# Performance work log

Hardware: AMD Instinct MI355X
Metric: run time of the kernel (lower is better)

## Reference

```python
import jax, jax.numpy as jnp
import numpy as np

B, S, D = 2, 2048, 2560
H, DH = 32, 80           # heads, head_size = D // H
RD = 32                  # rotary_dim (partial RoPE)
NI = 10240               # n_inner = 4 * n_embd
EPS = 1e-5
ROPE_BASE = 10000.0


def setup_inputs() -> dict:
    key = jax.random.key(0)
    ks = jax.random.split(key, 12)
    sd = 0.02
    inp = {
        "position_ids": jnp.broadcast_to(jnp.arange(S, dtype=jnp.int64), (B, S)),
        "hidden_states": jax.random.normal(ks[0], (B, S, D), jnp.float32),
        "ln_g": jnp.ones((D,), jnp.float32),
        "ln_b": jnp.zeros((D,), jnp.float32),
        "wqkv": jax.random.normal(ks[1], (D, 3 * D), jnp.float32) * sd,
        "bqkv": jnp.zeros((3 * D,), jnp.float32),
        "wout": jax.random.normal(ks[2], (D, D), jnp.float32) * sd,
        "bout": jnp.zeros((D,), jnp.float32),
        "wfc1": jax.random.normal(ks[3], (D, NI), jnp.float32) * sd,
        "bfc1": jnp.zeros((NI,), jnp.float32),
        "wfc2": jax.random.normal(ks[4], (NI, D), jnp.float32) * sd,
        "bfc2": jnp.zeros((D,), jnp.float32),
    }
    return inp


def _rope_neox(x, positions):
    # x: [B,S,H,DH]; apply neox-style rotary to first RD dims only
    half = RD // 2
    inv_freq = 1.0 / (ROPE_BASE ** (jnp.arange(0, RD, 2, dtype=jnp.float32) / RD))  # [half]
    ang = positions.astype(jnp.float32)[..., None] * inv_freq                        # [B,S,half]
    cos = jnp.cos(ang)[:, :, None, :]  # [B,S,1,half]
    sin = jnp.sin(ang)[:, :, None, :]
    x1 = x[..., :half]
    x2 = x[..., half:RD]
    rot = jnp.concatenate([x1 * cos - x2 * sin, x2 * cos + x1 * sin], axis=-1)
    return jnp.concatenate([rot, x[..., RD:]], axis=-1)


def reference(position_ids, hidden_states, ln_g, ln_b, wqkv, bqkv, wout, bout,
              wfc1, bfc1, wfc2, bfc2):
    residual = hidden_states
    # LayerNorm
    mu = jnp.mean(hidden_states, axis=-1, keepdims=True)
    var = jnp.mean(jnp.square(hidden_states - mu), axis=-1, keepdims=True)
    x = (hidden_states - mu) * jax.lax.rsqrt(var + EPS) * ln_g + ln_b

    # QKV projection
    qkv = x @ wqkv + bqkv
    q, k, v = jnp.split(qkv, 3, axis=-1)
    q = q.reshape(B, S, H, DH)
    k = k.reshape(B, S, H, DH)
    v = v.reshape(B, S, H, DH)

    # partial RoPE (neox style) on q and k
    q = _rope_neox(q, position_ids)
    k = _rope_neox(k, position_ids)

    # causal attention
    scale = DH ** -0.5
    scores = jnp.einsum("bqhd,bkhd->bhqk", q, k) * scale
    causal = jnp.tril(jnp.ones((S, S), jnp.bool_))
    scores = jnp.where(causal, scores, jnp.finfo(scores.dtype).min)
    probs = jax.nn.softmax(scores, axis=-1)
    attn = jnp.einsum("bhqk,bkhd->bqhd", probs, v).reshape(B, S, D)
    attn_out = attn @ wout + bout

    # MLP (gelu_new = tanh-approx gelu) on the SAME normed x (parallel residual)
    mlp = jax.nn.gelu(x @ wfc1 + bfc1, approximate=True) @ wfc2 + bfc2

    return attn_out + mlp + residual
```

## Files before the change

kernel.cpp:

```cpp
#include <hip/hip_runtime.h>

#define SS   2048
#define DD   2560
#define HH   32
#define DHH  80
#define DPAD 96
#define NII  10240
#define NTOK 4096

typedef __attribute__((ext_vector_type(8))) __bf16 bf16x8;
typedef __attribute__((ext_vector_type(4))) float  f32x4;

__device__ __forceinline__ float bf2f(unsigned short h) {
  union { unsigned u; float f; } c; c.u = ((unsigned)h) << 16; return c.f;
}
__device__ __forceinline__ unsigned short f2bf(float f) {
  union { float f; unsigned u; } c; c.f = f;
  unsigned r = c.u + 0x7FFFu + ((c.u >> 16) & 1u);
  return (unsigned short)(r >> 16);
}

__device__ __forceinline__ void gl_lds16(const void* gptr, void* lptr) {
  __builtin_amdgcn_global_load_lds((__attribute__((address_space(1))) void*)gptr,
                                   (__attribute__((address_space(3))) void*)lptr,
                                   16, 0, 0);
}

__global__ __launch_bounds__(256) void wt_transpose(const float* __restrict__ W,
                                                    unsigned short* __restrict__ Wt,
                                                    int K, int N) {
  __shared__ float tile[32][33];
  const int tx = threadIdx.x & 31, ty = threadIdx.x >> 5;
  const int n0 = blockIdx.x * 32, k0 = blockIdx.y * 32;
#pragma unroll
  for (int i = 0; i < 32; i += 8)
    tile[ty + i][tx] = W[(size_t)(k0 + ty + i) * N + n0 + tx];
  __syncthreads();
#pragma unroll
  for (int i = 0; i < 32; i += 8)
    Wt[(size_t)(n0 + ty + i) * K + k0 + tx] = f2bf(tile[tx][ty + i]);
}

__global__ __launch_bounds__(256) void ln_kernel(const float* __restrict__ X,
                                                 const float* __restrict__ G,
                                                 const float* __restrict__ Bb,
                                                 unsigned short* __restrict__ Xo) {
  const int row = blockIdx.x;
  const float4* xr = (const float4*)(X + (size_t)row * DD);
  float s = 0.f, ss = 0.f;
  for (int i = threadIdx.x; i < DD / 4; i += 256) {
    float4 v = xr[i];
    s  += v.x + v.y + v.z + v.w;
    ss += v.x * v.x + v.y * v.y + v.z * v.z + v.w * v.w;
  }
#pragma unroll
  for (int o = 32; o > 0; o >>= 1) { s += __shfl_down(s, o, 64); ss += __shfl_down(ss, o, 64); }
  __shared__ float red[8];
  const int w = threadIdx.x >> 6;
  if ((threadIdx.x & 63) == 0) { red[w] = s; red[4 + w] = ss; }
  __syncthreads();
  if (threadIdx.x == 0) {
    float ts  = red[0] + red[1] + red[2] + red[3];
    float tss = red[4] + red[5] + red[6] + red[7];
    float mu  = ts * (1.f / DD);
    float var = tss * (1.f / DD) - mu * mu;
    red[0] = mu; red[1] = rsqrtf(var + 1e-5f);
  }
  __syncthreads();
  const float mu = red[0], rstd = red[1];
  const float4* gr = (const float4*)G;
  const float4* br = (const float4*)Bb;
  for (int i = threadIdx.x; i < DD / 4; i += 256) {
    float4 v = xr[i], g = gr[i], b = br[i];
    ushort4 o;
    o.x = f2bf((v.x - mu) * rstd * g.x + b.x);
    o.y = f2bf((v.y - mu) * rstd * g.y + b.y);
    o.z = f2bf((v.z - mu) * rstd * g.z + b.z);
    o.w = f2bf((v.w - mu) * rstd * g.w + b.w);
    *(ushort4*)&Xo[(size_t)row * DD + i * 4] = o;
  }
}

__global__ __launch_bounds__(256) void rope_kernel(const unsigned short* __restrict__ qkv,
                                                   unsigned short* __restrict__ Qp,
                                                   unsigned short* __restrict__ Kp,
                                                   unsigned short* __restrict__ Vt) {
  const int tok = blockIdx.x;
  const int b = tok / SS, s = tok % SS;
  __shared__ float cs[16], sn[16];
  if (threadIdx.x < 16) {
    float inv = powf(10000.f, -(float)threadIdx.x / 16.f);
    float ang = (float)s * inv;
    cs[threadIdx.x] = cosf(ang);
    sn[threadIdx.x] = sinf(ang);
  }
  __syncthreads();
  const unsigned short* row = qkv + (size_t)tok * (3 * DD);
  for (int idx = threadIdx.x; idx < 2 * HH * DPAD; idx += 256) {
    const int which = idx / (HH * DPAD);
    const int rrem  = idx % (HH * DPAD);
    const int h = rrem / DPAD, d = rrem % DPAD;
    float val = 0.f;
    if (d < DHH) {
      const unsigned short* base = row + which * DD + h * DHH;
      if (d < 16) {
        float x1 = bf2f(base[d]), x2 = bf2f(base[d + 16]);
        val = x1 * cs[d] - x2 * sn[d];
      } else if (d < 32) {
        int i2 = d - 16;
        float x1 = bf2f(base[i2]), x2 = bf2f(base[d]);
        val = x2 * cs[i2] + x1 * sn[i2];
      } else {
        val = bf2f(base[d]);
      }
    }
    unsigned short* outp = which ? Kp : Qp;
    outp[(((size_t)b * HH + h) * SS + s) * DPAD + d] = f2bf(val);
  }
  for (int idx = threadIdx.x; idx < DD; idx += 256) {
    const int h = idx / DHH, d = idx % DHH;
    Vt[(((size_t)b * HH + h) * DHH + d) * SS + s] = row[2 * DD + idx];
  }
}

__global__ __launch_bounds__(128) void attn_kernel(const unsigned short* __restrict__ Qp,
                                                   const unsigned short* __restrict__ Kp,
                                                   const unsigned short* __restrict__ Vt,
                                                   unsigned short* __restrict__ O) {
  const int bid = blockIdx.x;
  const int bh = bid & 63;
  const int p = 63 - (bid >> 6);
  const int w = threadIdx.x >> 6;
  const int tile = p * 2 + w;
  const int lane = threadIdx.x & 63;
  const int lr = lane & 15, lg = lane >> 4;
  const int q0 = tile * 16;
  const unsigned short* Qh = Qp + (size_t)bh * SS * DPAD;
  const unsigned short* Kh = Kp + (size_t)bh * SS * DPAD;
  const unsigned short* Vh = Vt + (size_t)bh * DHH * SS;
  __shared__ __align__(16) char Plds[2][2048];
  char* Pb = Plds[w];

  bf16x8 qf[3];
#pragma unroll
  for (int c = 0; c < 3; ++c)
    qf[c] = *(const bf16x8*)&Qh[(size_t)(q0 + lr) * DPAD + c * 32 + lg * 8];

  f32x4 oacc[5];
#pragma unroll
  for (int d = 0; d < 5; ++d) oacc[d] = (f32x4){0.f, 0.f, 0.f, 0.f};
  float mrow[4], lrow[4];
#pragma unroll
  for (int r = 0; r < 4; ++r) { mrow[r] = -1e30f; lrow[r] = 0.f; }

  const float scl = 0.11180339887498949f;
  const int nt = q0 / 64 + 1;
  for (int t = 0; t < nt; ++t) {
    const int kv0 = t * 64;
    f32x4 s0 = (f32x4){0.f, 0.f, 0.f, 0.f};
    f32x4 s1 = (f32x4){0.f, 0.f, 0.f, 0.f};
    f32x4 s2 = (f32x4){0.f, 0.f, 0.f, 0.f};
    f32x4 s3 = (f32x4){0.f, 0.f, 0.f, 0.f};
#pragma unroll
    for (int c = 0; c < 3; ++c) {
      bf16x8 k0 = *(const bf16x8*)&Kh[(size_t)(kv0 +      lr) * DPAD + c * 32 + lg * 8];
      bf16x8 k1 = *(const bf16x8*)&Kh[(size_t)(kv0 + 16 + lr) * DPAD + c * 32 + lg * 8];
      bf16x8 k2 = *(const bf16x8*)&Kh[(size_t)(kv0 + 32 + lr) * DPAD + c * 32 + lg * 8];
      bf16x8 k3 = *(const bf16x8*)&Kh[(size_t)(kv0 + 48 + lr) * DPAD + c * 32 + lg * 8];
      s0 = __builtin_amdgcn_mfma_f32_16x16x32_bf16(qf[c], k0, s0, 0, 0, 0);
      s1 = __builtin_amdgcn_mfma_f32_16x16x32_bf16(qf[c], k1, s1, 0, 0, 0);
      s2 = __builtin_amdgcn_mfma_f32_16x16x32_bf16(qf[c], k2, s2, 0, 0, 0);
      s3 = __builtin_amdgcn_mfma_f32_16x16x32_bf16(qf[c], k3, s3, 0, 0, 0);
    }
    float pv0[4], pv1[4], pv2[4], pv3[4], mx[4];
    bool need = false;
#pragma unroll
    for (int r = 0; r < 4; ++r) {
      const int qr = q0 + lg * 4 + r;
      float a0 = (kv0 +      lr > qr) ? -1e30f : s0[r] * scl;
      float a1 = (kv0 + 16 + lr > qr) ? -1e30f : s1[r] * scl;
      float a2 = (kv0 + 32 + lr > qr) ? -1e30f : s2[r] * scl;
      float a3 = (kv0 + 48 + lr > qr) ? -1e30f : s3[r] * scl;
      pv0[r] = a0; pv1[r] = a1; pv2[r] = a2; pv3[r] = a3;
      float m = fmaxf(fmaxf(a0, a1), fmaxf(a2, a3));
#pragma unroll
      for (int mk = 1; mk < 16; mk <<= 1) m = fmaxf(m, __shfl_xor(m, mk, 64));
      mx[r] = m;
      need = need || (m > mrow[r] + 8.f);
    }
    if (__ballot(need)) {
#pragma unroll
      for (int r = 0; r < 4; ++r) {
        float mnew = fmaxf(mrow[r], mx[r]);
        float resc = __expf(mrow[r] - mnew);
        lrow[r] *= resc;
#pragma unroll
        for (int d = 0; d < 5; ++d) oacc[d][r] *= resc;
        mrow[r] = mnew;
      }
    }
#pragma unroll
    for (int r = 0; r < 4; ++r) {
      const int row = lg * 4 + r;
      const int swz = (row & 7) << 4;
      float p0 = __expf(pv0[r] - mrow[r]);
      float p1 = __expf(pv1[r] - mrow[r]);
      float p2 = __expf(pv2[r] - mrow[r]);
      float p3 = __expf(pv3[r] - mrow[r]);
      *(unsigned short*)(Pb + row * 128 + ((( 0 + lr) * 2) ^ swz)) = f2bf(p0);
      *(unsigned short*)(Pb + row * 128 + (((16 + lr) * 2) ^ swz)) = f2bf(p1);
      *(unsigned short*)(Pb + row * 128 + (((32 + lr) * 2) ^ swz)) = f2bf(p2);
      *(unsigned short*)(Pb + row * 128 + (((48 + lr) * 2) ^ swz)) = f2bf(p3);
      float rs = (p0 + p1) + (p2 + p3);
#pragma unroll
      for (int mk = 1; mk < 16; mk <<= 1) rs += __shfl_xor(rs, mk, 64);
      lrow[r] += rs;
    }
    asm volatile("s_waitcnt lgkmcnt(0)" ::: "memory");
    const int rswz = (lr & 7) << 4;
    bf16x8 pa0 = *(const bf16x8*)(Pb + lr * 128 + ((lg * 16) ^ rswz));
    bf16x8 pa1 = *(const bf16x8*)(Pb + lr * 128 + ((64 + lg * 16) ^ rswz));
#pragma unroll
    for (int d = 0; d < 5; ++d) {
      bf16x8 v0 = *(const bf16x8*)&Vh[(size_t)(d * 16 + lr) * SS + kv0 + lg * 8];
      bf16x8 v1 = *(const bf16x8*)&Vh[(size_t)(d * 16 + lr) * SS + kv0 + 32 + lg * 8];
      oacc[d] = __builtin_amdgcn_mfma_f32_16x16x32_bf16(pa0, v0, oacc[d], 0, 0, 0);
      oacc[d] = __builtin_amdgcn_mfma_f32_16x16x32_bf16(pa1, v1, oacc[d], 0, 0, 0);
    }
  }
  const int b = bh >> 5, h = bh & 31;
#pragma unroll
  for (int r = 0; r < 4; ++r) {
    const int qr = q0 + lg * 4 + r;
    const float inv = 1.f / lrow[r];
#pragma unroll
    for (int d = 0; d < 5; ++d)
      O[(size_t)(b * SS + qr) * DD + h * DHH + d * 16 + lr] = f2bf(oacc[d][r] * inv);
  }
}

__device__ __forceinline__ float gelu_f(float x) {
  float x3 = x * x * x;
  return 0.5f * x * (1.f + tanhf(0.7978845608028654f * (x + 0.044715f * x3)));
}

template <int MODE>
__global__ __launch_bounds__(512, 2) void gemm256(const unsigned short* __restrict__ A,
                                                  const unsigned short* __restrict__ Bt,
                                                  const float* __restrict__ bias,
                                                  void* __restrict__ Cout,
                                                  const unsigned short* __restrict__ addb,
                                                  const float* __restrict__ addf,
                                                  int M, int N, int K, int nbx) {
  __shared__ __align__(16) unsigned short smem[65536];
  char* ldsB = (char*)smem;

  const int nwg = gridDim.x;
  const int orig = blockIdx.x;
  const int qq = nwg >> 3, rr = nwg & 7;
  const int xcd = orig & 7, loc = orig >> 3;
  const int swz = (xcd < rr ? xcd * (qq + 1) : rr * (qq + 1) + (xcd - rr) * qq) + loc;
  const int by = swz / nbx, bx = swz % nbx;
  const int m0 = by * 256, n0 = bx * 256;

  const int tid = threadIdx.x;
  const int w = tid >> 6, lane = tid & 63;
  const int lr = lane & 15, lg = lane >> 4;
  const int wm = w & 1, wn = w >> 1;

  const int srow = w * 32 + (lane >> 2);
  const int sslot = ((lane & 3) ^ ((lane >> 3) & 3)) * 8;
  const unsigned short* aS0 = A  + (size_t)(m0 + srow) * K + sslot;
  const unsigned short* aS1 = A  + (size_t)(m0 + srow + 16) * K + sslot;
  const unsigned short* bS0 = Bt + (size_t)(n0 + srow) * K + sslot;
  const unsigned short* bS1 = Bt + (size_t)(n0 + srow + 16) * K + sslot;
  const int adest = w * 2048;

  const int fslot = ((lg ^ ((lr >> 1) & 3)) << 4);
  const int arow = wm * 128 + lr;
  const int brow = wn * 64 + lr;

  f32x4 acc[8][4];
#pragma unroll
  for (int i = 0; i < 8; ++i)
#pragma unroll
    for (int j = 0; j < 4; ++j) acc[i][j] = (f32x4){0.f, 0.f, 0.f, 0.f};

  const int nt = K >> 5;

#define STAGE_A(t)                                                        \
  { int _b = (t) & 3;                                                     \
    gl_lds16(aS0 + (size_t)(t) * 32, ldsB + _b * 16384 + adest);          \
    gl_lds16(aS1 + (size_t)(t) * 32, ldsB + _b * 16384 + adest + 1024); }
#define STAGE_B(t)                                                        \
  { int _b = (t) & 3;                                                     \
    gl_lds16(bS0 + (size_t)(t) * 32, ldsB + 65536 + _b * 16384 + adest);  \
    gl_lds16(bS1 + (size_t)(t) * 32, ldsB + 65536 + _b * 16384 + adest + 1024); }
#define LDA(t, m) (*(const bf16x8*)(ldsB + ((t) & 3) * 16384 + (arow + (m) * 16) * 64 + fslot))
#define LDB(t, n) (*(const bf16x8*)(ldsB + 65536 + ((t) & 3) * 16384 + (brow + (n) * 16) * 64 + fslot))

  STAGE_A(0); STAGE_B(0);
  STAGE_A(1); STAGE_B(1);
  STAGE_A(2); STAGE_B(2);
  asm volatile("s_waitcnt vmcnt(8)" ::: "memory");
  __builtin_amdgcn_s_barrier();
  __builtin_amdgcn_sched_barrier(0);

  for (int t = 0; t < nt; ++t) {
    bf16x8 b0 = LDB(t, 0), b1 = LDB(t, 1), b2 = LDB(t, 2), b3 = LDB(t, 3);
    bf16x8 a0 = LDA(t, 0), a1 = LDA(t, 1), a2 = LDA(t, 2), a3 = LDA(t, 3);
    if (t + 3 < nt) STAGE_A(t + 3);
    __builtin_amdgcn_s_barrier();
    __builtin_amdgcn_s_setprio(1);
    acc[0][0] = __builtin_amdgcn_mfma_f32_16x16x32_bf16(a0, b0, acc[0][0], 0, 0, 0);
    acc[0][1] = __builtin_amdgcn_mfma_f32_16x16x32_bf16(a0, b1, acc[0][1], 0, 0, 0);
    acc[0][2] = __builtin_amdgcn_mfma_f32_16x16x32_bf16(a0, b2, acc[0][2], 0, 0, 0);
    acc[0][3] = __builtin_amdgcn_mfma_f32_16x16x32_bf16(a0, b3, acc[0][3], 0, 0, 0);
    acc[1][0] = __builtin_amdgcn_mfma_f32_16x16x32_bf16(a1, b0, acc[1][0], 0, 0, 0);
    acc[1][1] = __builtin_amdgcn_mfma_f32_16x16x32_bf16(a1, b1, acc[1][1], 0, 0, 0);
    acc[1][2] = __builtin_amdgcn_mfma_f32_16x16x32_bf16(a1, b2, acc[1][2], 0, 0, 0);
    acc[1][3] = __builtin_amdgcn_mfma_f32_16x16x32_bf16(a1, b3, acc[1][3], 0, 0, 0);
    acc[2][0] = __builtin_amdgcn_mfma_f32_16x16x32_bf16(a2, b0, acc[2][0], 0, 0, 0);
    acc[2][1] = __builtin_amdgcn_mfma_f32_16x16x32_bf16(a2, b1, acc[2][1], 0, 0, 0);
    acc[2][2] = __builtin_amdgcn_mfma_f32_16x16x32_bf16(a2, b2, acc[2][2], 0, 0, 0);
    acc[2][3] = __builtin_amdgcn_mfma_f32_16x16x32_bf16(a2, b3, acc[2][3], 0, 0, 0);
    acc[3][0] = __builtin_amdgcn_mfma_f32_16x16x32_bf16(a3, b0, acc[3][0], 0, 0, 0);
    acc[3][1] = __builtin_amdgcn_mfma_f32_16x16x32_bf16(a3, b1, acc[3][1], 0, 0, 0);
    acc[3][2] = __builtin_amdgcn_mfma_f32_16x16x32_bf16(a3, b2, acc[3][2], 0, 0, 0);
    acc[3][3] = __builtin_amdgcn_mfma_f32_16x16x32_bf16(a3, b3, acc[3][3], 0, 0, 0);
    __builtin_amdgcn_s_setprio(0);
    __builtin_amdgcn_s_barrier();
    a0 = LDA(t, 4); a1 = LDA(t, 5); a2 = LDA(t, 6); a3 = LDA(t, 7);
    if (t + 3 < nt) STAGE_B(t + 3);
    __builtin_amdgcn_s_barrier();
    __builtin_amdgcn_s_setprio(1);
    acc[4][0] = __builtin_amdgcn_mfma_f32_16x16x32_bf16(a0, b0, acc[4][0], 0, 0, 0);
    acc[4][1] = __builtin_amdgcn_mfma_f32_16x16x32_bf16(a0, b1, acc[4][1], 0, 0, 0);
    acc[4][2] = __builtin_amdgcn_mfma_f32_16x16x32_bf16(a0, b2, acc[4][2], 0, 0, 0);
    acc[4][3] = __builtin_amdgcn_mfma_f32_16x16x32_bf16(a0, b3, acc[4][3], 0, 0, 0);
    acc[5][0] = __builtin_amdgcn_mfma_f32_16x16x32_bf16(a1, b0, acc[5][0], 0, 0, 0);
    acc[5][1] = __builtin_amdgcn_mfma_f32_16x16x32_bf16(a1, b1, acc[5][1], 0, 0, 0);
    acc[5][2] = __builtin_amdgcn_mfma_f32_16x16x32_bf16(a1, b2, acc[5][2], 0, 0, 0);
    acc[5][3] = __builtin_amdgcn_mfma_f32_16x16x32_bf16(a1, b3, acc[5][3], 0, 0, 0);
    acc[6][0] = __builtin_amdgcn_mfma_f32_16x16x32_bf16(a2, b0, acc[6][0], 0, 0, 0);
    acc[6][1] = __builtin_amdgcn_mfma_f32_16x16x32_bf16(a2, b1, acc[6][1], 0, 0, 0);
    acc[6][2] = __builtin_amdgcn_mfma_f32_16x16x32_bf16(a2, b2, acc[6][2], 0, 0, 0);
    acc[6][3] = __builtin_amdgcn_mfma_f32_16x16x32_bf16(a2, b3, acc[6][3], 0, 0, 0);
    acc[7][0] = __builtin_amdgcn_mfma_f32_16x16x32_bf16(a3, b0, acc[7][0], 0, 0, 0);
    acc[7][1] = __builtin_amdgcn_mfma_f32_16x16x32_bf16(a3, b1, acc[7][1], 0, 0, 0);
    acc[7][2] = __builtin_amdgcn_mfma_f32_16x16x32_bf16(a3, b2, acc[7][2], 0, 0, 0);
    acc[7][3] = __builtin_amdgcn_mfma_f32_16x16x32_bf16(a3, b3, acc[7][3], 0, 0, 0);
    __builtin_amdgcn_s_setprio(0);
    const int rem = nt - 2 - t;
    if (rem >= 2)      asm volatile("s_waitcnt vmcnt(8)" ::: "memory");
    else if (rem == 1) asm volatile("s_waitcnt vmcnt(4)" ::: "memory");
    else               asm volatile("s_waitcnt vmcnt(0)" ::: "memory");
    __builtin_amdgcn_s_barrier();
    __builtin_amdgcn_sched_barrier(0);
  }
#undef STAGE_A
#undef STAGE_B
#undef LDA
#undef LDB

#pragma unroll
  for (int m = 0; m < 8; ++m) {
    const int rb = m0 + wm * 128 + m * 16 + lg * 4;
#pragma unroll
    for (int n = 0; n < 4; ++n) {
      const int col = n0 + wn * 64 + n * 16 + lr;
      const float bv = bias[col];
#pragma unroll
      for (int r = 0; r < 4; ++r) {
        const size_t idx = (size_t)(rb + r) * N + col;
        float v = acc[m][n][r] + bv;
        if (MODE == 2) v = gelu_f(v);
        if (MODE == 3) {
          ((float*)Cout)[idx] = v + bf2f(addb[idx]) + addf[idx];
        } else {
          ((unsigned short*)Cout)[idx] = f2bf(v);
        }
      }
    }
  }
}

extern "C" void kernel_launch(void* const* d_in, const int* in_sizes, int n_in,
                              void* d_out, int out_size, void* d_ws, size_t ws_size,
                              hipStream_t stream) {
  (void)in_sizes; (void)n_in; (void)out_size; (void)ws_size;
  const float* hidden = (const float*)d_in[1];
  const float* ln_g = (const float*)d_in[2];
  const float* ln_b = (const float*)d_in[3];
  const float* wqkv = (const float*)d_in[4];
  const float* bqkv = (const float*)d_in[5];
  const float* wout = (const float*)d_in[6];
  const float* bout = (const float*)d_in[7];
  const float* wfc1 = (const float*)d_in[8];
  const float* bfc1 = (const float*)d_in[9];
  const float* wfc2 = (const float*)d_in[10];
  const float* bfc2 = (const float*)d_in[11];
  float* out = (float*)d_out;

  char* ws = (char*)d_ws;
  size_t off = 0;
  auto alloc = [&](size_t bytes) -> void* {
    void* p = ws + off;
    off += (bytes + 255) & ~(size_t)255;
    return p;
  };
  unsigned short* wqkvT = (unsigned short*)alloc((size_t)3 * DD * DD * 2);
  unsigned short* woutT = (unsigned short*)alloc((size_t)DD * DD * 2);
  unsigned short* wfc1T = (unsigned short*)alloc((size_t)NII * DD * 2);
  unsigned short* wfc2T = (unsigned short*)alloc((size_t)DD * NII * 2);
  unsigned short* xln   = (unsigned short*)alloc((size_t)NTOK * DD * 2);
  unsigned short* regA  = (unsigned short*)alloc((size_t)NTOK * NII * 2);
  unsigned short* Qp    = (unsigned short*)alloc((size_t)2 * HH * SS * DPAD * 2);
  unsigned short* Kp    = (unsigned short*)alloc((size_t)2 * HH * SS * DPAD * 2);
  unsigned short* Vt    = (unsigned short*)alloc((size_t)2 * HH * DHH * SS * 2);
  unsigned short* Obuf  = (unsigned short*)alloc((size_t)NTOK * DD * 2);
  unsigned short* qkvbuf   = regA;
  unsigned short* h1       = regA;
  unsigned short* attnproj = Qp;

  wt_transpose<<<dim3(3 * DD / 32, DD / 32), 256, 0, stream>>>(wqkv, wqkvT, DD, 3 * DD);
  wt_transpose<<<dim3(DD / 32, DD / 32), 256, 0, stream>>>(wout, woutT, DD, DD);
  wt_transpose<<<dim3(NII / 32, DD / 32), 256, 0, stream>>>(wfc1, wfc1T, DD, NII);
  wt_transpose<<<dim3(DD / 32, NII / 32), 256, 0, stream>>>(wfc2, wfc2T, NII, DD);
  ln_kernel<<<NTOK, 256, 0, stream>>>(hidden, ln_g, ln_b, xln);
  gemm256<0><<<dim3((3 * DD / 256) * (NTOK / 256)), 512, 0, stream>>>(
      xln, wqkvT, bqkv, qkvbuf, nullptr, nullptr, NTOK, 3 * DD, DD, 3 * DD / 256);
  rope_kernel<<<NTOK, 256, 0, stream>>>(qkvbuf, Qp, Kp, Vt);
  attn_kernel<<<dim3(4096), 128, 0, stream>>>(Qp, Kp, Vt, Obuf);
  gemm256<0><<<dim3((DD / 256) * (NTOK / 256)), 512, 0, stream>>>(
      Obuf, woutT, bout, attnproj, nullptr, nullptr, NTOK, DD, DD, DD / 256);
  gemm256<2><<<dim3((NII / 256) * (NTOK / 256)), 512, 0, stream>>>(
      xln, wfc1T, bfc1, h1, nullptr, nullptr, NTOK, NII, DD, NII / 256);
  gemm256<3><<<dim3((DD / 256) * (NTOK / 256)), 512, 0, stream>>>(
      h1, wfc2T, bfc2, out, attnproj, hidden, NTOK, DD, NII, DD / 256);
}
```

Measured before the change: 1.326 ms.

## Restructure GEMM main loop to K=64 steps with double-buffered half-tile staging

Reworks the 256x256 bf16 GEMM pipeline so each loop iteration covers a 64-wide K slice as two 32-wide halves, held in two LDS buffers instead of a four-deep ring of 32-wide stages. Global-to-LDS loads for the next halves are interleaved between the four MFMA phases. Loop overhead and waitcnt branching are roughly halved per unit of K. In exchange, prefetch depth changes from three stages ahead to about one and a half, which may expose more memory latency. LDS usage stays at 128 KB.

```diff
diff --git a/kernel.cpp b/kernel.cpp
--- a/kernel.cpp
+++ b/kernel.cpp
@@ -252,8 +252,7 @@
                                                   const unsigned short* __restrict__ addb,
                                                   const float* __restrict__ addf,
                                                   int M, int N, int K, int nbx) {
-  __shared__ __align__(16) unsigned short smem[65536];
-  char* ldsB = (char*)smem;
+  __shared__ __align__(16) char lds[131072];
 
   const int nwg = gridDim.x;
   const int orig = blockIdx.x;
@@ -269,16 +268,14 @@
   const int wm = w & 1, wn = w >> 1;
 
   const int srow = w * 32 + (lane >> 2);
-  const int sslot = ((lane & 3) ^ ((lane >> 3) & 3)) * 8;
-  const unsigned short* aS0 = A  + (size_t)(m0 + srow) * K + sslot;
-  const unsigned short* aS1 = A  + (size_t)(m0 + srow + 16) * K + sslot;
-  const unsigned short* bS0 = Bt + (size_t)(n0 + srow) * K + sslot;
-  const unsigned short* bS1 = Bt + (size_t)(n0 + srow + 16) * K + sslot;
-  const int adest = w * 2048;
-
-  const int fslot = ((lg ^ ((lr >> 1) & 3)) << 4);
-  const int arow = wm * 128 + lr;
-  const int brow = wn * 64 + lr;
+  const int skc  = ((lane & 3) ^ ((lane >> 3) & 3)) * 8;
+  const unsigned short* aSrc = A  + (size_t)(m0 + srow) * K + skc;
+  const unsigned short* bSrc = Bt + (size_t)(n0 + srow) * K + skc;
+  const int sdst = w * 2048;
+
+  const int fsw = (lg ^ ((lr >> 1) & 3)) << 4;
+  const int arowb = (wm * 128 + lr) * 64;
+  const int browb = (wn * 64 + lr) * 64;
 
   f32x4 acc[8][4];
 #pragma unroll
@@ -286,82 +283,79 @@
 #pragma unroll
     for (int j = 0; j < 4; ++j) acc[i][j] = (f32x4){0.f, 0.f, 0.f, 0.f};
 
-  const int nt = K >> 5;
-
-#define STAGE_A(t)                                                        \
-  { int _b = (t) & 3;                                                     \
-    gl_lds16(aS0 + (size_t)(t) * 32, ldsB + _b * 16384 + adest);          \
-    gl_lds16(aS1 + (size_t)(t) * 32, ldsB + _b * 16384 + adest + 1024); }
-#define STAGE_B(t)                                                        \
-  { int _b = (t) & 3;                                                     \
-    gl_lds16(bS0 + (size_t)(t) * 32, ldsB + 65536 + _b * 16384 + adest);  \
-    gl_lds16(bS1 + (size_t)(t) * 32, ldsB + 65536 + _b * 16384 + adest + 1024); }
-#define LDA(t, m) (*(const bf16x8*)(ldsB + ((t) & 3) * 16384 + (arow + (m) * 16) * 64 + fslot))
-#define LDB(t, n) (*(const bf16x8*)(ldsB + 65536 + ((t) & 3) * 16384 + (brow + (n) * 16) * 64 + fslot))
-
-  STAGE_A(0); STAGE_B(0);
-  STAGE_A(1); STAGE_B(1);
-  STAGE_A(2); STAGE_B(2);
-  asm volatile("s_waitcnt vmcnt(8)" ::: "memory");
+  const int nt = K >> 6;
+
+#define STG(srcp, kt, h, base)                                          \
+  { const unsigned short* _g = (srcp) + (size_t)(kt) * 64 + (h) * 32;   \
+    gl_lds16(_g, lds + (base) + sdst);                                  \
+    gl_lds16(_g + (size_t)16 * K, lds + (base) + sdst + 1024); }
+#define LDAF(base, h, m) (*(const bf16x8*)(lds + (base) + (h) * 16384 + arowb + (m) * 1024 + fsw))
+#define LDBF(base, h, n) (*(const bf16x8*)(lds + (base) + (h) * 16384 + browb + (n) * 1024 + fsw))
+#define MFMA16(lo)                                                      \
+  _Pragma("unroll") for (int i = 0; i < 4; ++i)                         \
+  _Pragma("unroll") for (int j = 0; j < 4; ++j)                         \
+    acc[(lo) + i][j] = __builtin_amdgcn_mfma_f32_16x16x32_bf16(av[i], bv[j], acc[(lo) + i][j], 0, 0, 0);
+
+  STG(aSrc, 0, 0, 0);
+  STG(bSrc, 0, 0, 65536);
+  STG(aSrc, 0, 1, 16384);
+  STG(bSrc, 0, 1, 65536 + 16384);
+  STG(aSrc, 1, 0, 32768);
+  STG(bSrc, 1, 0, 65536 + 32768);
+  asm volatile("s_waitcnt vmcnt(4)" ::: "memory");
   __builtin_amdgcn_s_barrier();
   __builtin_amdgcn_sched_barrier(0);
 
-  for (int t = 0; t < nt; ++t) {
-    bf16x8 b0 = LDB(t, 0), b1 = LDB(t, 1), b2 = LDB(t, 2), b3 = LDB(t, 3);
-    bf16x8 a0 = LDA(t, 0), a1 = LDA(t, 1), a2 = LDA(t, 2), a3 = LDA(t, 3);
-    if (t + 3 < nt) STAGE_A(t + 3);
+  for (int k = 0; k < nt; ++k) {
+    const int c = k & 1;
+    const int cAb = c * 32768,         cBb = 65536 + c * 32768;
+    const int nAb = (c ^ 1) * 32768,   nBb = 65536 + (c ^ 1) * 32768;
+    bf16x8 av[4], bv[4];
+#pragma unroll
+    for (int i = 0; i < 4; ++i) av[i] = LDAF(cAb, 0, i);
+#pragma unroll
+    for (int j = 0; j < 4; ++j) bv[j] = LDBF(cBb, 0, j);
+    if (k + 1 < nt) STG(aSrc, k + 1, 1, nAb + 16384);
     __builtin_amdgcn_s_barrier();
     __builtin_amdgcn_s_setprio(1);
-    acc[0][0] = __builtin_amdgcn_mfma_f32_16x16x32_bf16(a0, b0, acc[0][0], 0, 0, 0);
-    acc[0][1] = __builtin_amdgcn_mfma_f32_16x16x32_bf16(a0, b1, acc[0][1], 0, 0, 0);
-    acc[0][2] = __builtin_amdgcn_mfma_f32_16x16x32_bf16(a0, b2, acc[0][2], 0, 0, 0);
-    acc[0][3] = __builtin_amdgcn_mfma_f32_16x16x32_bf16(a0, b3, acc[0][3], 0, 0, 0);
-    acc[1][0] = __builtin_amdgcn_mfma_f32_16x16x32_bf16(a1, b0, acc[1][0], 0, 0, 0);
-    acc[1][1] = __builtin_amdgcn_mfma_f32_16x16x32_bf16(a1, b1, acc[1][1], 0, 0, 0);
-    acc[1][2] = __builtin_amdgcn_mfma_f32_16x16x32_bf16(a1, b2, acc[1][2], 0, 0, 0);
-    acc[1][3] = __builtin_amdgcn_mfma_f32_16x16x32_bf16(a1, b3, acc[1][3], 0, 0, 0);
-    acc[2][0] = __builtin_amdgcn_mfma_f32_16x16x32_bf16(a2, b0, acc[2][0], 0, 0, 0);
-    acc[2][1] = __builtin_amdgcn_mfma_f32_16x16x32_bf16(a2, b1, acc[2][1], 0, 0, 0);
-    acc[2][2] = __builtin_amdgcn_mfma_f32_16x16x32_bf16(a2, b2, acc[2][2], 0, 0, 0);
-    acc[2][3] = __builtin_amdgcn_mfma_f32_16x16x32_bf16(a2, b3, acc[2][3], 0, 0, 0);
-    acc[3][0] = __builtin_amdgcn_mfma_f32_16x16x32_bf16(a3, b0, acc[3][0], 0, 0, 0);
-    acc[3][1] = __builtin_amdgcn_mfma_f32_16x16x32_bf16(a3, b1, acc[3][1], 0, 0, 0);
-    acc[3][2] = __builtin_amdgcn_mfma_f32_16x16x32_bf16(a3, b2, acc[3][2], 0, 0, 0);
-    acc[3][3] = __builtin_amdgcn_mfma_f32_16x16x32_bf16(a3, b3, acc[3][3], 0, 0, 0);
+    MFMA16(0);
     __builtin_amdgcn_s_setprio(0);
     __builtin_amdgcn_s_barrier();
-    a0 = LDA(t, 4); a1 = LDA(t, 5); a2 = LDA(t, 6); a3 = LDA(t, 7);
-    if (t + 3 < nt) STAGE_B(t + 3);
+#pragma unroll
+    for (int i = 0; i < 4; ++i) av[i] = LDAF(cAb, 0, 4 + i);
+    if (k + 1 < nt) STG(bSrc, k + 1, 1, nBb + 16384);
     __builtin_amdgcn_s_barrier();
     __builtin_amdgcn_s_setprio(1);
-    acc[4][0] = __builtin_amdgcn_mfma_f32_16x16x32_bf16(a0, b0, acc[4][0], 0, 0, 0);
-    acc[4][1] = __builtin_amdgcn_mfma_f32_16x16x32_bf16(a0, b1, acc[4][1], 0, 0, 0);
-    acc[4][2] = __builtin_amdgcn_mfma_f32_16x16x32_bf16(a0, b2, acc[4][2], 0, 0, 0);
-    acc[4][3] = __builtin_amdgcn_mfma_f32_16x16x32_bf16(a0, b3, acc[4][3], 0, 0, 0);
-    acc[5][0] = __builtin_amdgcn_mfma_f32_16x16x32_bf16(a1, b0, acc[5][0], 0, 0, 0);
-    acc[5][1] = __builtin_amdgcn_mfma_f32_16x16x32_bf16(a1, b1, acc[5][1], 0, 0, 0);
-    acc[5][2] = __builtin_amdgcn_mfma_f32_16x16x32_bf16(a1, b2, acc[5][2], 0, 0, 0);
-    acc[5][3] = __builtin_amdgcn_mfma_f32_16x16x32_bf16(a1, b3, acc[5][3], 0, 0, 0);
-    acc[6][0] = __builtin_amdgcn_mfma_f32_16x16x32_bf16(a2, b0, acc[6][0], 0, 0, 0);
-    acc[6][1] = __builtin_amdgcn_mfma_f32_16x16x32_bf16(a2, b1, acc[6][1], 0, 0, 0);
-    acc[6][2] = __builtin_amdgcn_mfma_f32_16x16x32_bf16(a2, b2, acc[6][2], 0, 0, 0);
-    acc[6][3] = __builtin_amdgcn_mfma_f32_16x16x32_bf16(a2, b3, acc[6][3], 0, 0, 0);
-    acc[7][0] = __builtin_amdgcn_mfma_f32_16x16x32_bf16(a3, b0, acc[7][0], 0, 0, 0);
-    acc[7][1] = __builtin_amdgcn_mfma_f32_16x16x32_bf16(a3, b1, acc[7][1], 0, 0, 0);
-    acc[7][2] = __builtin_amdgcn_mfma_f32_16x16x32_bf16(a3, b2, acc[7][2], 0, 0, 0);
-    acc[7][3] = __builtin_amdgcn_mfma_f32_16x16x32_bf16(a3, b3, acc[7][3], 0, 0, 0);
+    MFMA16(4);
     __builtin_amdgcn_s_setprio(0);
-    const int rem = nt - 2 - t;
-    if (rem >= 2)      asm volatile("s_waitcnt vmcnt(8)" ::: "memory");
-    else if (rem == 1) asm volatile("s_waitcnt vmcnt(4)" ::: "memory");
-    else               asm volatile("s_waitcnt vmcnt(0)" ::: "memory");
+    __builtin_amdgcn_s_barrier();
+#pragma unroll
+    for (int i = 0; i < 4; ++i) av[i] = LDAF(cAb, 1, i);
+#pragma unroll
+    for (int j = 0; j < 4; ++j) bv[j] = LDBF(cBb, 1, j);
+    if (k + 2 < nt) STG(aSrc, k + 2, 0, cAb);
+    __builtin_amdgcn_s_barrier();
+    __builtin_amdgcn_s_setprio(1);
+    MFMA16(0);
+    __builtin_amdgcn_s_setprio(0);
+    __builtin_amdgcn_s_barrier();
+#pragma unroll
+    for (int i = 0; i < 4; ++i) av[i] = LDAF(cAb, 1, 4 + i);
+    if (k + 2 < nt) STG(bSrc, k + 2, 0, cBb);
+    __builtin_amdgcn_s_barrier();
+    __builtin_amdgcn_s_setprio(1);
+    MFMA16(4);
+    __builtin_amdgcn_s_setprio(0);
+    const int rem = nt - 1 - k;
+    if (rem >= 2) asm volatile("s_waitcnt vmcnt(4)" ::: "memory");
+    else          asm volatile("s_waitcnt vmcnt(0)" ::: "memory");
     __builtin_amdgcn_s_barrier();
     __builtin_amdgcn_sched_barrier(0);
   }
-#undef STAGE_A
-#undef STAGE_B
-#undef LDA
-#undef LDB
+#undef STG
+#undef LDAF
+#undef LDBF
+#undef MFMA16
 
 #pragma unroll
   for (int m = 0; m < 8; ++m) {
```

Result: no change. 1.313 ms (-1.0%).
